# Optimization experiments

Hardware: AMD Instinct MI355X
Metric: run time of the kernel (lower is better)

Reference implementation:

```python
import jax, jax.numpy as jnp
import numpy as np

VOCAB = 50257
EMB = 256
HID = 512
NCLS = 50257


def setup_inputs() -> dict:
    key = jax.random.key(0)
    ks = jax.random.split(key, 6)
    x = jax.random.randint(ks[0], (64, 512), 0, VOCAB, dtype=jnp.int32)
    emb_weight = jax.random.normal(ks[1], (VOCAB, EMB), dtype=jnp.float32) * 0.01
    # torch Linear: weight [out_features, in_features], bias [out_features]
    lim_w = 1.0 / np.sqrt(EMB + HID)
    W_weight = jax.random.uniform(ks[2], (4 * HID, EMB + HID), jnp.float32, -lim_w, lim_w)
    W_bias = jax.random.uniform(ks[3], (4 * HID,), jnp.float32, -lim_w, lim_w)
    lim_fc = 1.0 / np.sqrt(HID)
    fc_weight = jax.random.uniform(ks[4], (NCLS, HID), jnp.float32, -lim_fc, lim_fc)
    fc_bias = jax.random.uniform(ks[5], (NCLS,), jnp.float32, -lim_fc, lim_fc)
    return {"x": x, "emb_weight": emb_weight, "W_weight": W_weight,
            "W_bias": W_bias, "fc_weight": fc_weight, "fc_bias": fc_bias}


def reference(x, emb_weight, W_weight, W_bias, fc_weight, fc_bias):
    B, S = x.shape
    H = W_weight.shape[0] // 4
    embedded = emb_weight[x]                     # [B, S, E]
    Wx = W_weight[:, :EMB]                       # [4H, E]
    Wh = W_weight[:, EMB:]                       # [4H, H]

    def step(carry, x_t):
        h, C = carry
        gates = x_t @ Wx.T + h @ Wh.T + W_bias   # [B, 4H]
        f, i, o, c_tilde = jnp.split(gates, 4, axis=1)
        f = jax.nn.sigmoid(f)
        i = jax.nn.sigmoid(i)
        o = jax.nn.sigmoid(o)
        c_tilde = jnp.tanh(c_tilde)
        C_new = f * C + i * c_tilde
        h_new = o * jnp.tanh(C_new)
        return (h_new, C_new), None

    h0 = jnp.zeros((B, H), embedded.dtype)
    C0 = jnp.zeros((B, H), embedded.dtype)
    (h, _), _ = jax.lax.scan(step, (h0, C0), jnp.swapaxes(embedded, 0, 1))
    return h @ fc_weight.T + fc_bias             # [B, num_classes]
```

## Files before the change

### kernel.cpp

```cpp
#include <hip/hip_runtime.h>
#include <stdint.h>

#define EMBD   256
#define HID    512
#define KTOT   768
#define NCLS   50257
#define STEPS  512

#define NGROUP 8
#define GB     8
#define BPG    32
#define HS     16
#define UPITCH 776
#define RP     129

typedef float f32x4  __attribute__((ext_vector_type(4)));
typedef short bf16x8 __attribute__((ext_vector_type(8)));
typedef unsigned long long u64;

__device__ __forceinline__ unsigned bf16_rne(float f) {
  unsigned u = __float_as_uint(f);
  return (u + 0x7FFFu + ((u >> 16) & 1u)) >> 16;
}
__device__ __forceinline__ float bf16_to_f32(unsigned b) {
  return __uint_as_float(b << 16);
}

__global__ void emb_prep(const int* __restrict__ x, const float* __restrict__ emb,
                         unsigned* __restrict__ emb_hl) {
  int base = blockIdx.x * 4;
  int k = threadIdx.x;
  for (int it = 0; it < 4; ++it) {
    int tok = base + it;
    int id = x[tok];
    float w = emb[(size_t)id * EMBD + k];
    unsigned hb = bf16_rne(w);
    unsigned lb = bf16_rne(w - bf16_to_f32(hb));
    emb_hl[(size_t)tok * EMBD + k] = hb | (lb << 16);
  }
}

__global__ __launch_bounds__(512, 2) void lstm_persist(
    const float* __restrict__ Ww, const float* __restrict__ Wb,
    const unsigned* __restrict__ emb_hl,
    u64* __restrict__ hbuf,
    unsigned short* __restrict__ h_hi, unsigned short* __restrict__ h_lo)
{
  __shared__ __align__(16) unsigned short u_hi[16 * UPITCH];
  __shared__ __align__(16) unsigned short u_lo[16 * UPITCH];
  __shared__ __align__(16) float red[32 * RP];

  const int tid  = threadIdx.x;
  const int wave = tid >> 6;
  const int lane = tid & 63;
  const int g = blockIdx.x & 7;
  const int s = blockIdx.x >> 3;

  for (int i = tid; i < 16 * UPITCH; i += 512) { u_hi[i] = 0; u_lo[i] = 0; }

  const int cn = lane & 15;
  const int qk = (lane >> 4) * 8;
  bf16x8 whi[3][4], wlo[3][4];
#pragma unroll
  for (int i = 0; i < 3; ++i) {
    int kt = wave * 3 + i;
    int k0 = kt * 32 + qk;
#pragma unroll
    for (int nt = 0; nt < 4; ++nt) {
      int row = nt * 512 + s * HS + cn;
      const float* src = Ww + (size_t)row * KTOT + k0;
      float4 w0 = *(const float4*)src;
      float4 w1 = *(const float4*)(src + 4);
      float wv[8] = {w0.x, w0.y, w0.z, w0.w, w1.x, w1.y, w1.z, w1.w};
#pragma unroll
      for (int j = 0; j < 8; ++j) {
        unsigned hb = bf16_rne(wv[j]);
        unsigned lb = bf16_rne(wv[j] - bf16_to_f32(hb));
        whi[i][nt][j] = (short)hb;
        wlo[i][nt][j] = (short)lb;
      }
    }
  }

  const float bias = Wb[(lane >> 4) * 512 + s * HS + (lane & 15)];

  float Cst = 0.0f;

  const unsigned* embg = emb_hl + (size_t)(g * GB) * STEPS * EMBD;
  u64* hg = hbuf + (size_t)g * 2 * GB * HID;

  __syncthreads();

  for (int step = 0; step < STEPS; ++step) {
    {
      int f0 = tid * 4;
      int b = f0 >> 8, k0 = f0 & 255;
      uint4 v = *(const uint4*)(embg + ((size_t)b * STEPS + step) * EMBD + k0);
      unsigned h01 = (v.x & 0xFFFFu) | ((v.y & 0xFFFFu) << 16);
      unsigned h23 = (v.z & 0xFFFFu) | ((v.w & 0xFFFFu) << 16);
      unsigned l01 = (v.x >> 16) | (v.y & 0xFFFF0000u);
      unsigned l23 = (v.z >> 16) | (v.w & 0xFFFF0000u);
      *(uint2*)&u_hi[b * UPITCH + k0] = make_uint2(h01, h23);
      *(uint2*)&u_lo[b * UPITCH + k0] = make_uint2(l01, l23);
    }
    {
      const u64* hp = hg + ((size_t)(step & 1) * GB + wave) * HID;
      u64 v[8];
      const unsigned want = (unsigned)step;
      while (true) {
        bool ok = true;
#pragma unroll
        for (int j = 0; j < 8; ++j)
          v[j] = __hip_atomic_load(&hp[j * 64 + lane], __ATOMIC_RELAXED,
                                   __HIP_MEMORY_SCOPE_AGENT);
#pragma unroll
        for (int j = 0; j < 8; ++j)
          ok &= ((unsigned)(v[j] >> 32) == want);
        if (ok) break;
        __builtin_amdgcn_s_sleep(1);
      }
#pragma unroll
      for (int j = 0; j < 8; ++j) {
        unsigned w32 = (unsigned)v[j];
        u_hi[wave * UPITCH + EMBD + j * 64 + lane] = (unsigned short)(w32 & 0xFFFFu);
        u_lo[wave * UPITCH + EMBD + j * 64 + lane] = (unsigned short)(w32 >> 16);
      }
    }
    __syncthreads();

    f32x4 acc[4] = {{0.f,0.f,0.f,0.f},{0.f,0.f,0.f,0.f},
                    {0.f,0.f,0.f,0.f},{0.f,0.f,0.f,0.f}};
#pragma unroll
    for (int i = 0; i < 3; ++i) {
      int k0 = (wave * 3 + i) * 32 + qk;
      int m = lane & 15;
      bf16x8 ahi = *(const bf16x8*)&u_hi[m * UPITCH + k0];
      bf16x8 alo = *(const bf16x8*)&u_lo[m * UPITCH + k0];
#pragma unroll
      for (int nt = 0; nt < 4; ++nt) {
        acc[nt] = __builtin_amdgcn_mfma_f32_16x16x32_bf16(ahi, whi[i][nt], acc[nt], 0, 0, 0);
        acc[nt] = __builtin_amdgcn_mfma_f32_16x16x32_bf16(ahi, wlo[i][nt], acc[nt], 0, 0, 0);
        acc[nt] = __builtin_amdgcn_mfma_f32_16x16x32_bf16(alo, whi[i][nt], acc[nt], 0, 0, 0);
      }
    }
    if (lane < 32) {
#pragma unroll
      for (int nt = 0; nt < 4; ++nt)
        *(f32x4*)&red[(wave * 4 + nt) * RP + lane * 4] = acc[nt];
    }
    __syncthreads();

    float gsum = bias;
    {
      int tq = lane >> 4;
      int rbase = ((((wave >> 2) << 4) | (lane & 15)) << 2) + (wave & 3);
#pragma unroll
      for (int w = 0; w < 8; ++w)
        gsum += red[(w * 4 + tq) * RP + rbase];
    }

    float scl = (lane >= 48) ? 2.0f : 1.0f;
    float y = 1.0f / (1.0f + __expf(-gsum * scl));
    float act = (lane >= 48) ? (2.0f * y - 1.0f) : y;
    float ig = __shfl(act, lane + 16);
    float og = __shfl(act, lane + 32);
    float cg = __shfl(act, lane + 48);
    if (lane < 16) {
      Cst = act * Cst + ig * cg;
      float t2 = 1.0f / (1.0f + __expf(-2.0f * Cst));
      float hv = og * (2.0f * t2 - 1.0f);
      unsigned hb = bf16_rne(hv);
      unsigned lb = bf16_rne(hv - bf16_to_f32(hb));
      u64 pack = ((u64)(unsigned)(step + 1) << 32) | (u64)(hb | (lb << 16));
      __hip_atomic_store(
          &hg[((size_t)((step + 1) & 1) * GB + wave) * HID + s * HS + lane],
          pack, __ATOMIC_RELAXED, __HIP_MEMORY_SCOPE_AGENT);
      if (step == STEPS - 1) {
        int m = g * GB + wave, k = s * HS + lane;
        h_hi[m * HID + k] = (unsigned short)hb;
        h_lo[m * HID + k] = (unsigned short)lb;
      }
    }
  }
}

__device__ __forceinline__ void cvt8(const float4& a, const float4& b,
                                     bf16x8& hi, bf16x8& lo) {
  float v[8] = {a.x, a.y, a.z, a.w, b.x, b.y, b.z, b.w};
#pragma unroll
  for (int j = 0; j < 8; ++j) {
    unsigned hb = bf16_rne(v[j]);
    hi[j] = (short)hb;
    lo[j] = (short)bf16_rne(v[j] - bf16_to_f32(hb));
  }
}

__global__ __launch_bounds__(512) void fc_mfma(
    const unsigned short* __restrict__ h_hi, const unsigned short* __restrict__ h_lo,
    const float* __restrict__ fcw, const float* __restrict__ fcb,
    float* __restrict__ out)
{
  const int tid = threadIdx.x, wave = tid >> 6, lane = tid & 63;
  const int cn = lane & 15;
  const int qk = (lane >> 4) * 8;
  const int cls  = blockIdx.x * 128 + wave * 16 + cn;
  const int clsc = cls < NCLS ? cls : NCLS - 1;

  f32x4 acc[4] = {{0.f,0.f,0.f,0.f},{0.f,0.f,0.f,0.f},
                  {0.f,0.f,0.f,0.f},{0.f,0.f,0.f,0.f}};
#pragma unroll 2
  for (int kt = 0; kt < 16; ++kt) {
    int k0 = kt * 32 + qk;
    const float* bp = fcw + (size_t)clsc * HID + k0;
    float4 b0 = *(const float4*)bp;
    float4 b1 = *(const float4*)(bp + 4);
    bf16x8 bhi, blo;
    cvt8(b0, b1, bhi, blo);
#pragma unroll
    for (int mt = 0; mt < 4; ++mt) {
      bf16x8 ahi = *(const bf16x8*)&h_hi[(size_t)(mt * 16 + cn) * HID + k0];
      bf16x8 alo = *(const bf16x8*)&h_lo[(size_t)(mt * 16 + cn) * HID + k0];
      acc[mt] = __builtin_amdgcn_mfma_f32_16x16x32_bf16(ahi, bhi, acc[mt], 0, 0, 0);
      acc[mt] = __builtin_amdgcn_mfma_f32_16x16x32_bf16(ahi, blo, acc[mt], 0, 0, 0);
      acc[mt] = __builtin_amdgcn_mfma_f32_16x16x32_bf16(alo, bhi, acc[mt], 0, 0, 0);
    }
  }
  if (cls < NCLS) {
    float bias = fcb[cls];
#pragma unroll
    for (int mt = 0; mt < 4; ++mt)
#pragma unroll
      for (int j = 0; j < 4; ++j) {
        int m = mt * 16 + (lane >> 4) * 4 + j;
        out[(size_t)m * NCLS + cls] = acc[mt][j] + bias;
      }
  }
}

extern "C" void kernel_launch(void* const* d_in, const int* in_sizes, int n_in,
                              void* d_out, int out_size, void* d_ws, size_t ws_size,
                              hipStream_t stream) {
  const int*   x   = (const int*)d_in[0];
  const float* emb = (const float*)d_in[1];
  const float* Ww  = (const float*)d_in[2];
  const float* Wb  = (const float*)d_in[3];
  const float* fcw = (const float*)d_in[4];
  const float* fcb = (const float*)d_in[5];
  float* out = (float*)d_out;

  char* ws = (char*)d_ws;
  u64*            hbuf   = (u64*)ws;
  unsigned short* h_hi   = (unsigned short*)(ws + 524288);
  unsigned short* h_lo   = (unsigned short*)(ws + 524288 + 65536);
  unsigned*       emb_hl = (unsigned*)(ws + 524288 + 131072);

  hipMemsetAsync(hbuf, 0, 524288, stream);

  emb_prep<<<8192, 256, 0, stream>>>(x, emb, emb_hl);

  void* args[] = { (void*)&Ww, (void*)&Wb, (void*)&emb_hl,
                   (void*)&hbuf, (void*)&h_hi, (void*)&h_lo };
  hipLaunchCooperativeKernel((void*)lstm_persist, dim3(256), dim3(512),
                             args, 0, stream);

  fc_mfma<<<(NCLS + 127) / 128, 512, 0, stream>>>(h_hi, h_lo, fcw, fcb, out);
}
```

Before: 1.386 ms.

## Poll hidden-state exchange through XCC-local cache when all group blocks share an XCC

At kernel start, each block records its XCC id, followed by a grid sync. Every block then checks whether all blocks of each group land on the same XCC. If they do, the per-step hidden-state polling uses sc0 loads that can hit the shared L2 instead of device-scope atomic loads, with a device-scope load every fourth round as a fallback. The store is issued twice, once with sc0 and once atomically. This aims to cut the latency of the inter-block handoff on the recurrence, but it relies on the hardware's block-to-XCC placement and on coherence behaviour that the code does not guarantee.

```diff
diff --git a/kernel.cpp b/kernel.cpp
--- a/kernel.cpp
+++ b/kernel.cpp
@@ -1,5 +1,8 @@
 #include <hip/hip_runtime.h>
+#include <hip/hip_cooperative_groups.h>
 #include <stdint.h>
+
+namespace cg = cooperative_groups;
 
 #define EMBD   256
 #define HID    512
@@ -44,7 +47,8 @@
     const float* __restrict__ Ww, const float* __restrict__ Wb,
     const unsigned* __restrict__ emb_hl,
     u64* __restrict__ hbuf,
-    unsigned short* __restrict__ h_hi, unsigned short* __restrict__ h_lo)
+    unsigned short* __restrict__ h_hi, unsigned short* __restrict__ h_lo,
+    unsigned* __restrict__ xcc_tab)
 {
   __shared__ __align__(16) unsigned short u_hi[16 * UPITCH];
   __shared__ __align__(16) unsigned short u_lo[16 * UPITCH];
@@ -88,6 +92,21 @@
 
   const unsigned* embg = emb_hl + (size_t)(g * GB) * STEPS * EMBD;
   u64* hg = hbuf + (size_t)g * 2 * GB * HID;
+
+  unsigned xcc = 0;
+  asm volatile("s_getreg_b32 %0, hwreg(HW_REG_XCC_ID)" : "=s"(xcc));
+  if (tid == 0)
+    __hip_atomic_store(&xcc_tab[blockIdx.x], xcc, __ATOMIC_RELAXED,
+                       __HIP_MEMORY_SCOPE_AGENT);
+  cg::this_grid().sync();
+  bool xfast = true;
+  for (int i = 0; i < (int)gridDim.x; ++i) {
+    unsigned a = __hip_atomic_load(&xcc_tab[i], __ATOMIC_RELAXED,
+                                   __HIP_MEMORY_SCOPE_AGENT);
+    unsigned b = __hip_atomic_load(&xcc_tab[i & 7], __ATOMIC_RELAXED,
+                                   __HIP_MEMORY_SCOPE_AGENT);
+    xfast &= (a == b);
+  }
 
   __syncthreads();
 
@@ -105,18 +124,38 @@
     }
     {
       const u64* hp = hg + ((size_t)(step & 1) * GB + wave) * HID;
+      const u64* ap = hp + lane;
       u64 v[8];
       const unsigned want = (unsigned)step;
+      int round = 0;
       while (true) {
+        if (xfast && (round & 3) != 3) {
+          asm volatile(
+            "global_load_dwordx2 %0, %8, off sc0\n\t"
+            "global_load_dwordx2 %1, %8, off offset:512 sc0\n\t"
+            "global_load_dwordx2 %2, %8, off offset:1024 sc0\n\t"
+            "global_load_dwordx2 %3, %8, off offset:1536 sc0\n\t"
+            "global_load_dwordx2 %4, %8, off offset:2048 sc0\n\t"
+            "global_load_dwordx2 %5, %8, off offset:2560 sc0\n\t"
+            "global_load_dwordx2 %6, %8, off offset:3072 sc0\n\t"
+            "global_load_dwordx2 %7, %8, off offset:3584 sc0\n\t"
+            "s_waitcnt vmcnt(0)"
+            : "=v"(v[0]), "=v"(v[1]), "=v"(v[2]), "=v"(v[3]),
+              "=v"(v[4]), "=v"(v[5]), "=v"(v[6]), "=v"(v[7])
+            : "v"(ap)
+            : "memory");
+        } else {
+#pragma unroll
+          for (int j = 0; j < 8; ++j)
+            v[j] = __hip_atomic_load(&hp[j * 64 + lane], __ATOMIC_RELAXED,
+                                     __HIP_MEMORY_SCOPE_AGENT);
+        }
         bool ok = true;
-#pragma unroll
-        for (int j = 0; j < 8; ++j)
-          v[j] = __hip_atomic_load(&hp[j * 64 + lane], __ATOMIC_RELAXED,
-                                   __HIP_MEMORY_SCOPE_AGENT);
 #pragma unroll
         for (int j = 0; j < 8; ++j)
           ok &= ((unsigned)(v[j] >> 32) == want);
         if (ok) break;
+        ++round;
         __builtin_amdgcn_s_sleep(1);
       }
 #pragma unroll
@@ -164,17 +203,19 @@
     float act = (lane >= 48) ? (2.0f * y - 1.0f) : y;
     float ig = __shfl(act, lane + 16);
     float og = __shfl(act, lane + 32);
-    float cg = __shfl(act, lane + 48);
+    float cg_ = __shfl(act, lane + 48);
     if (lane < 16) {
-      Cst = act * Cst + ig * cg;
+      Cst = act * Cst + ig * cg_;
       float t2 = 1.0f / (1.0f + __expf(-2.0f * Cst));
       float hv = og * (2.0f * t2 - 1.0f);
       unsigned hb = bf16_rne(hv);
       unsigned lb = bf16_rne(hv - bf16_to_f32(hb));
       u64 pack = ((u64)(unsigned)(step + 1) << 32) | (u64)(hb | (lb << 16));
-      __hip_atomic_store(
-          &hg[((size_t)((step + 1) & 1) * GB + wave) * HID + s * HS + lane],
-          pack, __ATOMIC_RELAXED, __HIP_MEMORY_SCOPE_AGENT);
+      u64* sp = &hg[((size_t)((step + 1) & 1) * GB + wave) * HID + s * HS + lane];
+      if (xfast)
+        asm volatile("global_store_dwordx2 %0, %1, off sc0"
+                     :: "v"(sp), "v"(pack) : "memory");
+      __hip_atomic_store(sp, pack, __ATOMIC_RELAXED, __HIP_MEMORY_SCOPE_AGENT);
       if (step == STEPS - 1) {
         int m = g * GB + wave, k = s * HS + lane;
         h_hi[m * HID + k] = (unsigned short)hb;
@@ -252,14 +293,15 @@
   u64*            hbuf   = (u64*)ws;
   unsigned short* h_hi   = (unsigned short*)(ws + 524288);
   unsigned short* h_lo   = (unsigned short*)(ws + 524288 + 65536);
-  unsigned*       emb_hl = (unsigned*)(ws + 524288 + 131072);
+  unsigned*       xcc_tab= (unsigned*)(ws + 524288 + 131072);
+  unsigned*       emb_hl = (unsigned*)(ws + 524288 + 131072 + 4096);
 
   hipMemsetAsync(hbuf, 0, 524288, stream);
 
   emb_prep<<<8192, 256, 0, stream>>>(x, emb, emb_hl);
 
   void* args[] = { (void*)&Ww, (void*)&Wb, (void*)&emb_hl,
-                   (void*)&hbuf, (void*)&h_hi, (void*)&h_lo };
+                   (void*)&hbuf, (void*)&h_hi, (void*)&h_lo, (void*)&xcc_tab };
   hipLaunchCooperativeKernel((void*)lstm_persist, dim3(256), dim3(512),
                              args, 0, stream);
 
```

Measured after the change: 2.210 ms. +59.4%, slower.
